# Optimization experiments

Measured on AMD Instinct MI355X. Metric: run time of the kernel, lower is better.

## Reference

```python
import jax, jax.numpy as jnp
import numpy as np
from jax import lax

ROWS, COLS, HID = 5, 5, 4
N = ROWS * COLS
NUM_NEURONS = 128


def _nbr_indices(i, direction):
    # Faithful to get_neighbor_hidden, including the row-wrap behavior of
    # 'col-1'/'col+1' (no column bounds check in the original code).
    row, col = divmod(i, COLS)
    up = (row - 1) * COLS + col
    dn = (row + 1) * COLS + col
    lf = row * COLS + col - 1
    rt = row * COLS + col + 1
    return [up, dn, lf, rt] if direction == 'f' else [up, dn, rt, lf]


def _gather_neighbors(h, idxs):
    # h: (N, bs, HID); returns (bs, 4) of the 4th hidden feature per neighbor
    bs = h.shape[1]
    cols_list = [h[j][:, 3] if 0 <= j < N else jnp.zeros((bs,), h.dtype) for j in idxs]
    return jnp.stack(cols_list, axis=1)


def _make_step(Wx, Wh, Wn, b, direction):
    # One timestep: nodes updated sequentially (node i sees already-updated
    # up/left neighbors within the same timestep, matching the torch loop).
    def step(carry, x_t):  # x_t: (N, bs)
        h, c = carry  # each (N, bs, HID)
        for i in range(N):
            nb = _gather_neighbors(h, _nbr_indices(i, direction))  # (bs,4)
            gates = x_t[i][:, None] @ Wx + h[i] @ Wh + nb @ Wn + b  # (bs,4H)
            ig, fg, og, cc = jnp.split(gates, 4, axis=1)
            nc = jax.nn.sigmoid(fg) * c[i] + jax.nn.sigmoid(ig) * jnp.tanh(cc)
            nh = jax.nn.sigmoid(og) * jnp.tanh(nc)
            h = h.at[i].set(nh)
            c = c.at[i].set(nc)
        return (h, c), None
    return step


def _forward(x, h0f, c0f, h0b, c0b, Wx_f, Wh_f, Wn_f, b_f,
             Wx_b, Wh_b, Wn_b, b_b, W_ff, b_ff, W_out, b_out):
    bs = x.shape[0]
    x_seq = jnp.transpose(x, (2, 1, 0))  # (T, N, bs)
    (hf, cf), _ = lax.scan(_make_step(Wx_f, Wh_f, Wn_f, b_f, 'f'), (h0f, c0f), x_seq)
    (hb, cb), _ = lax.scan(_make_step(Wx_b, Wh_b, Wn_b, b_b, 'b'), (h0b, c0b), x_seq[::-1])
    H_fwd = jnp.transpose(hf, (1, 0, 2))  # (bs, N, HID)
    H_bwd = jnp.transpose(hb, (1, 0, 2))
    H = jnp.concatenate([H_fwd, H_bwd], axis=2).reshape(bs, -1)  # (bs, 200)
    ff = jax.nn.sigmoid(H @ W_ff + b_ff)
    return jax.nn.softmax(ff @ W_out + b_out, axis=1)


def setup_inputs() -> dict:
    key = jax.random.key(0)
    ks = jax.random.split(key, 16)
    bs, T = 8192, 128
    d = {}
    d['x'] = jax.random.normal(ks[0], (bs, N, T), jnp.float32)
    for nm, k in zip(['h0f', 'c0f', 'h0b', 'c0b'], ks[1:5]):
        d[nm] = jax.random.normal(k, (N, bs, HID), jnp.float32) * 0.01
    def lin(k, i, o):
        return jax.random.normal(k, (i, o), jnp.float32) * (1.0 / np.sqrt(i))
    d['Wx_f'] = lin(ks[5], 1, 4 * HID)
    d['Wh_f'] = lin(ks[6], HID, 4 * HID)
    d['Wn_f'] = lin(ks[7], 4, 4 * HID)
    d['b_f'] = jnp.zeros((4 * HID,), jnp.float32)
    d['Wx_b'] = lin(ks[8], 1, 4 * HID)
    d['Wh_b'] = lin(ks[9], HID, 4 * HID)
    d['Wn_b'] = lin(ks[10], 4, 4 * HID)
    d['b_b'] = jnp.zeros((4 * HID,), jnp.float32)
    d['W_ff'] = lin(ks[11], N * 2 * HID, NUM_NEURONS)
    d['b_ff'] = jnp.zeros((NUM_NEURONS,), jnp.float32)
    d['W_out'] = lin(ks[12], NUM_NEURONS, 2)
    d['b_out'] = jnp.zeros((2,), jnp.float32)
    return d


def reference(x, h0f, c0f, h0b, c0b, Wx_f, Wh_f, Wn_f, b_f,
              Wx_b, Wh_b, Wn_b, b_b, W_ff, b_ff, W_out, b_out):
    return _forward(x, h0f, c0f, h0b, c0b, Wx_f, Wh_f, Wn_f, b_f,
                    Wx_b, Wh_b, Wn_b, b_b, W_ff, b_ff, W_out, b_out)
```

## Files before the change

kernel.cpp:

```cpp
#include <hip/hip_runtime.h>
#include <stddef.h>

#define BS 8192
#define NNODE 25
#define TT 128
#define LOG2E 1.4426950408889634f

typedef float v2f __attribute__((ext_vector_type(2)));

__device__ __forceinline__ float ex2(float x) { return __builtin_amdgcn_exp2f(x); }
__device__ __forceinline__ float rcp_(float x) { return __builtin_amdgcn_rcpf(x); }

__device__ float g_xT[(size_t)TT * NNODE * BS];
__device__ float g_hf[NNODE * BS * 4];
__device__ float g_hb[NNODE * BS * 4];

template <int K>
__device__ __forceinline__ float bcast4(float v) {
  int s = __builtin_bit_cast(int, v);
  int r = __builtin_amdgcn_update_dpp(0, s, (K * 0x55), 0xF, 0xF, true);
  return __builtin_bit_cast(float, r);
}

__device__ __forceinline__ void acc2(v2f& A, v2f& B, float s, v2f wa, v2f wb) {
  v2f sv = {s, s};
  A = __builtin_elementwise_fma(sv, wa, A);
  B = __builtin_elementwise_fma(sv, wb, B);
}

__global__ __launch_bounds__(256) void transpose_x(const float* __restrict__ x) {
  __shared__ float tile[32][33];
  const int i = blockIdx.z;
  const int b0 = blockIdx.x * 32;
  const int t0 = blockIdx.y * 32;
  const int tx = threadIdx.x;
  const int ty = threadIdx.y;
#pragma unroll
  for (int j = 0; j < 4; ++j) {
    int bl = ty + j * 8;
    tile[bl][tx] = x[((size_t)(b0 + bl) * NNODE + i) * TT + (t0 + tx)];
  }
  __syncthreads();
#pragma unroll
  for (int j = 0; j < 4; ++j) {
    int tl = ty + j * 8;
    g_xT[((size_t)(t0 + tl) * NNODE + i) * BS + (b0 + tx)] = tile[tx][tl];
  }
}

__global__ __launch_bounds__(256, 1) void rnn_kernel(
    const float* __restrict__ h0f, const float* __restrict__ c0f,
    const float* __restrict__ h0b, const float* __restrict__ c0b,
    const float* __restrict__ Wxf, const float* __restrict__ Whf,
    const float* __restrict__ Wnf, const float* __restrict__ bf,
    const float* __restrict__ Wxb, const float* __restrict__ Whb,
    const float* __restrict__ Wnb, const float* __restrict__ bb_) {
  const int dir = blockIdx.y;
  const int d = threadIdx.x & 3;
  const int b = blockIdx.x * 64 + (threadIdx.x >> 2);

  const float* Wx = dir ? Wxb : Wxf;
  const float* Wh = dir ? Whb : Whf;
  const float* Wn = dir ? Wnb : Wnf;
  const float* Bb = dir ? bb_ : bf;
  const float* h0 = dir ? h0b : h0f;
  const float* c0 = dir ? c0b : c0f;

  const int cI = d, cF = 4 + d, cO = 8 + d, cC = 12 + d;
  const float sS = -LOG2E, sC = 2.0f * LOG2E;

  v2f wA[9], wB[9];
  {
    wA[0] = v2f{sS * Wx[cI], sS * Wx[cF]};
    wB[0] = v2f{sS * Wx[cO], sC * Wx[cC]};
#pragma unroll
    for (int k = 0; k < 4; ++k) {
      wA[1 + k] = v2f{sS * Wh[k * 16 + cI], sS * Wh[k * 16 + cF]};
      wB[1 + k] = v2f{sS * Wh[k * 16 + cO], sC * Wh[k * 16 + cC]};
    }
    const int nrow[4] = {0, 1, dir ? 3 : 2, dir ? 2 : 3};
#pragma unroll
    for (int k = 0; k < 4; ++k) {
      wA[5 + k] = v2f{sS * Wn[nrow[k] * 16 + cI], sS * Wn[nrow[k] * 16 + cF]};
      wB[5 + k] = v2f{sS * Wn[nrow[k] * 16 + cO], sC * Wn[nrow[k] * 16 + cC]};
    }
  }
  const v2f bA = {sS * Bb[cI], sS * Bb[cF]};
  const v2f bB = {sS * Bb[cO], sC * Bb[cC]};

  float h[NNODE], c[NNODE], b3[NNODE];
#pragma unroll
  for (int i = 0; i < NNODE; ++i) {
    h[i] = h0[(i * BS + b) * 4 + d];
    c[i] = c0[(i * BS + b) * 4 + d];
    b3[i] = bcast4<3>(h[i]);
  }

  const float* xbase = g_xT + ((size_t)(dir ? (TT - 1) : 0) * NNODE * BS);
  const ptrdiff_t xstep = dir ? -(ptrdiff_t)(NNODE * BS) : (ptrdiff_t)(NNODE * BS);

  for (int t = 0; t < TT; ++t) {
    float xv[NNODE];
#pragma unroll
    for (int i = 0; i < NNODE; ++i) xv[i] = xbase[(size_t)i * BS + b];

#pragma unroll
    for (int i = 0; i < NNODE; ++i) {
      const float f0 = bcast4<0>(h[i]);
      const float f1 = bcast4<1>(h[i]);
      const float f2 = bcast4<2>(h[i]);

      v2f A = bA, B = bB;
      acc2(A, B, xv[i], wA[0], wB[0]);
      acc2(A, B, f0, wA[1], wB[1]);
      acc2(A, B, f1, wA[2], wB[2]);
      acc2(A, B, f2, wA[3], wB[3]);
      acc2(A, B, b3[i], wA[4], wB[4]);
      if (i >= 5) acc2(A, B, b3[i - 5], wA[5], wB[5]);
      if (i < 20) acc2(A, B, b3[i + 5], wA[6], wB[6]);
      if (i >= 1) acc2(A, B, b3[i - 1], wA[7], wB[7]);
      if (i < 24) acc2(A, B, b3[i + 1], wA[8], wB[8]);

      const float Ei = ex2(A.x);
      const float Ef = ex2(A.y);
      const float Eo = ex2(B.x);
      const float Ec = ex2(B.y);
      const float Di = 1.0f + Ei;
      const float Df = 1.0f + Ef;
      const float P = Di * (Ec + 1.0f);
      const float num = fmaf(c[i], P, (Ec - 1.0f) * Df);
      const float nc = num * rcp_(Df * P);
      const float En = ex2(-2.0f * LOG2E * nc);
      const float hn = (1.0f - En) * rcp_((1.0f + En) * (1.0f + Eo));
      c[i] = nc;
      h[i] = hn;
      b3[i] = bcast4<3>(hn);
    }
    xbase += xstep;
  }

  float* ho = dir ? g_hb : g_hf;
#pragma unroll
  for (int i = 0; i < NNODE; ++i) ho[(i * BS + b) * 4 + d] = h[i];
}

__global__ __launch_bounds__(128) void ff_kernel(
    const float* __restrict__ Wff, const float* __restrict__ bff,
    const float* __restrict__ Wout, const float* __restrict__ bout,
    float* __restrict__ out) {
  __shared__ float Hs[8][200];
  __shared__ float ffs[8][129];
  const int tid = threadIdx.x;
  const int b0 = blockIdx.x * 8;

  for (int idx = tid; idx < 8 * 200; idx += 128) {
    const int bb = idx / 200;
    const int k = idx - bb * 200;
    const int i = k >> 3;
    const int dd = k & 7;
    const int b = b0 + bb;
    Hs[bb][k] = (dd < 4) ? g_hf[(i * BS + b) * 4 + dd]
                         : g_hb[(i * BS + b) * 4 + (dd - 4)];
  }
  __syncthreads();

  float acc[8];
  const float bv = bff[tid];
#pragma unroll
  for (int bb = 0; bb < 8; ++bb) acc[bb] = bv;
  for (int k = 0; k < 200; ++k) {
    const float w = Wff[k * 128 + tid];
#pragma unroll
    for (int bb = 0; bb < 8; ++bb) acc[bb] = fmaf(Hs[bb][k], w, acc[bb]);
  }
#pragma unroll
  for (int bb = 0; bb < 8; ++bb)
    ffs[bb][tid] = rcp_(1.0f + ex2(-LOG2E * acc[bb]));
  __syncthreads();

  if (tid < 8) {
    float z0 = bout[0], z1 = bout[1];
    for (int n = 0; n < 128; ++n) {
      const float f = ffs[tid][n];
      z0 = fmaf(f, Wout[n * 2 + 0], z0);
      z1 = fmaf(f, Wout[n * 2 + 1], z1);
    }
    const float m = fmaxf(z0, z1);
    const float e0 = ex2(LOG2E * (z0 - m)), e1 = ex2(LOG2E * (z1 - m));
    const float s = rcp_(e0 + e1);
    out[(size_t)(b0 + tid) * 2 + 0] = e0 * s;
    out[(size_t)(b0 + tid) * 2 + 1] = e1 * s;
  }
}

extern "C" void kernel_launch(void* const* d_in, const int* in_sizes, int n_in,
                              void* d_out, int out_size, void* d_ws, size_t ws_size,
                              hipStream_t stream) {
  (void)in_sizes; (void)n_in; (void)out_size; (void)d_ws; (void)ws_size;
  const float* x    = (const float*)d_in[0];
  const float* h0f  = (const float*)d_in[1];
  const float* c0f  = (const float*)d_in[2];
  const float* h0b  = (const float*)d_in[3];
  const float* c0b  = (const float*)d_in[4];
  const float* Wxf  = (const float*)d_in[5];
  const float* Whf  = (const float*)d_in[6];
  const float* Wnf  = (const float*)d_in[7];
  const float* bf   = (const float*)d_in[8];
  const float* Wxb  = (const float*)d_in[9];
  const float* Whb  = (const float*)d_in[10];
  const float* Wnb  = (const float*)d_in[11];
  const float* bb   = (const float*)d_in[12];
  const float* Wff  = (const float*)d_in[13];
  const float* bff  = (const float*)d_in[14];
  const float* Wout = (const float*)d_in[15];
  const float* bout = (const float*)d_in[16];
  float* out = (float*)d_out;

  transpose_x<<<dim3(256, 4, 25), dim3(32, 8), 0, stream>>>(x);
  rnn_kernel<<<dim3(128, 2), dim3(256), 0, stream>>>(
      h0f, c0f, h0b, c0b, Wxf, Whf, Wnf, bf, Wxb, Whb, Wnb, bb);
  ff_kernel<<<dim3(1024), dim3(128), 0, stream>>>(Wff, bff, Wout, bout, out);
}
```

Baseline: 590.9 us.

## Drop transpose kernel; read x directly in RNN with paired-timestep vector loads

Removes the separate transpose_x pass and its global scratch buffer, so the RNN kernel reads x in its original (bs, N, T) layout. Each thread loads two consecutive timesteps per node as one float2 and processes two timesteps per outer iteration, with a templated direction. This saves a full read and write of the 105 MB input but makes the RNN loads uncoalesced: the four lanes sharing a batch row hit the same address and neighbouring batch rows are N*T floats apart.

```diff
diff --git a/kernel.cpp b/kernel.cpp
--- a/kernel.cpp
+++ b/kernel.cpp
@@ -11,7 +11,6 @@
 __device__ __forceinline__ float ex2(float x) { return __builtin_amdgcn_exp2f(x); }
 __device__ __forceinline__ float rcp_(float x) { return __builtin_amdgcn_rcpf(x); }
 
-__device__ float g_xT[(size_t)TT * NNODE * BS];
 __device__ float g_hf[NNODE * BS * 4];
 __device__ float g_hb[NNODE * BS * 4];
 
@@ -28,120 +27,108 @@
   B = __builtin_elementwise_fma(sv, wb, B);
 }
 
-__global__ __launch_bounds__(256) void transpose_x(const float* __restrict__ x) {
-  __shared__ float tile[32][33];
-  const int i = blockIdx.z;
-  const int b0 = blockIdx.x * 32;
-  const int t0 = blockIdx.y * 32;
-  const int tx = threadIdx.x;
-  const int ty = threadIdx.y;
-#pragma unroll
-  for (int j = 0; j < 4; ++j) {
-    int bl = ty + j * 8;
-    tile[bl][tx] = x[((size_t)(b0 + bl) * NNODE + i) * TT + (t0 + tx)];
-  }
-  __syncthreads();
-#pragma unroll
-  for (int j = 0; j < 4; ++j) {
-    int tl = ty + j * 8;
-    g_xT[((size_t)(t0 + tl) * NNODE + i) * BS + (b0 + tx)] = tile[tx][tl];
-  }
+template <int DIR>
+__device__ __forceinline__ void rnn_run(
+    int d, int b, const float* __restrict__ x,
+    const float* __restrict__ h0, const float* __restrict__ c0,
+    const float* __restrict__ Wx, const float* __restrict__ Wh,
+    const float* __restrict__ Wn, const float* __restrict__ Bb,
+    float* __restrict__ ho) {
+  const int cI = d, cF = 4 + d, cO = 8 + d, cC = 12 + d;
+  const float sS = -LOG2E, sC = 2.0f * LOG2E;
+
+  v2f wA[9], wB[9];
+  wA[0] = v2f{sS * Wx[cI], sS * Wx[cF]};
+  wB[0] = v2f{sS * Wx[cO], sC * Wx[cC]};
+#pragma unroll
+  for (int k = 0; k < 4; ++k) {
+    wA[1 + k] = v2f{sS * Wh[k * 16 + cI], sS * Wh[k * 16 + cF]};
+    wB[1 + k] = v2f{sS * Wh[k * 16 + cO], sC * Wh[k * 16 + cC]};
+  }
+  const int nrow[4] = {0, 1, DIR ? 3 : 2, DIR ? 2 : 3};
+#pragma unroll
+  for (int k = 0; k < 4; ++k) {
+    wA[5 + k] = v2f{sS * Wn[nrow[k] * 16 + cI], sS * Wn[nrow[k] * 16 + cF]};
+    wB[5 + k] = v2f{sS * Wn[nrow[k] * 16 + cO], sC * Wn[nrow[k] * 16 + cC]};
+  }
+  const v2f bA = {sS * Bb[cI], sS * Bb[cF]};
+  const v2f bB = {sS * Bb[cO], sC * Bb[cC]};
+
+  float h[NNODE], c[NNODE], b3[NNODE];
+#pragma unroll
+  for (int i = 0; i < NNODE; ++i) {
+    h[i] = h0[(i * BS + b) * 4 + d];
+    c[i] = c0[(i * BS + b) * 4 + d];
+    b3[i] = bcast4<3>(h[i]);
+  }
+
+  const float* xrow = x + (size_t)b * (NNODE * TT);
+
+  for (int blk = 0; blk < TT / 2; ++blk) {
+    const int tbase = DIR ? (TT - 2 - 2 * blk) : (2 * blk);
+    v2f xv[NNODE];
+#pragma unroll
+    for (int i = 0; i < NNODE; ++i)
+      xv[i] = *(const v2f*)(xrow + i * TT + tbase);
+
+#pragma unroll
+    for (int k = 0; k < 2; ++k) {
+#pragma unroll
+      for (int i = 0; i < NNODE; ++i) {
+        const float xval =
+            (((DIR ? (1 - k) : k) == 0) ? xv[i].x : xv[i].y);
+        const float f0 = bcast4<0>(h[i]);
+        const float f1 = bcast4<1>(h[i]);
+        const float f2 = bcast4<2>(h[i]);
+
+        v2f A = bA, B = bB;
+        acc2(A, B, xval, wA[0], wB[0]);
+        acc2(A, B, f0, wA[1], wB[1]);
+        acc2(A, B, f1, wA[2], wB[2]);
+        acc2(A, B, f2, wA[3], wB[3]);
+        acc2(A, B, b3[i], wA[4], wB[4]);
+        if (i >= 5) acc2(A, B, b3[i - 5], wA[5], wB[5]);
+        if (i < 20) acc2(A, B, b3[i + 5], wA[6], wB[6]);
+        if (i >= 1) acc2(A, B, b3[i - 1], wA[7], wB[7]);
+        if (i < 24) acc2(A, B, b3[i + 1], wA[8], wB[8]);
+
+        const float Ei = ex2(A.x);
+        const float Ef = ex2(A.y);
+        const float Eo = ex2(B.x);
+        const float Ec = ex2(B.y);
+        const float Di = 1.0f + Ei;
+        const float Df = 1.0f + Ef;
+        const float P = Di * (Ec + 1.0f);
+        const float num = fmaf(c[i], P, (Ec - 1.0f) * Df);
+        const float nc = num * rcp_(Df * P);
+        const float En = ex2(-2.0f * LOG2E * nc);
+        const float hn = (1.0f - En) * rcp_((1.0f + En) * (1.0f + Eo));
+        c[i] = nc;
+        h[i] = hn;
+        b3[i] = bcast4<3>(hn);
+      }
+    }
+  }
+
+#pragma unroll
+  for (int i = 0; i < NNODE; ++i) ho[(i * BS + b) * 4 + d] = h[i];
 }
 
 __global__ __launch_bounds__(256, 1) void rnn_kernel(
+    const float* __restrict__ x,
     const float* __restrict__ h0f, const float* __restrict__ c0f,
     const float* __restrict__ h0b, const float* __restrict__ c0b,
     const float* __restrict__ Wxf, const float* __restrict__ Whf,
     const float* __restrict__ Wnf, const float* __restrict__ bf,
     const float* __restrict__ Wxb, const float* __restrict__ Whb,
     const float* __restrict__ Wnb, const float* __restrict__ bb_) {
-  const int dir = blockIdx.y;
   const int d = threadIdx.x & 3;
   const int b = blockIdx.x * 64 + (threadIdx.x >> 2);
-
-  const float* Wx = dir ? Wxb : Wxf;
-  const float* Wh = dir ? Whb : Whf;
-  const float* Wn = dir ? Wnb : Wnf;
-  const float* Bb = dir ? bb_ : bf;
-  const float* h0 = dir ? h0b : h0f;
-  const float* c0 = dir ? c0b : c0f;
-
-  const int cI = d, cF = 4 + d, cO = 8 + d, cC = 12 + d;
-  const float sS = -LOG2E, sC = 2.0f * LOG2E;
-
-  v2f wA[9], wB[9];
-  {
-    wA[0] = v2f{sS * Wx[cI], sS * Wx[cF]};
-    wB[0] = v2f{sS * Wx[cO], sC * Wx[cC]};
-#pragma unroll
-    for (int k = 0; k < 4; ++k) {
-      wA[1 + k] = v2f{sS * Wh[k * 16 + cI], sS * Wh[k * 16 + cF]};
-      wB[1 + k] = v2f{sS * Wh[k * 16 + cO], sC * Wh[k * 16 + cC]};
-    }
-    const int nrow[4] = {0, 1, dir ? 3 : 2, dir ? 2 : 3};
-#pragma unroll
-    for (int k = 0; k < 4; ++k) {
-      wA[5 + k] = v2f{sS * Wn[nrow[k] * 16 + cI], sS * Wn[nrow[k] * 16 + cF]};
-      wB[5 + k] = v2f{sS * Wn[nrow[k] * 16 + cO], sC * Wn[nrow[k] * 16 + cC]};
-    }
-  }
-  const v2f bA = {sS * Bb[cI], sS * Bb[cF]};
-  const v2f bB = {sS * Bb[cO], sC * Bb[cC]};
-
-  float h[NNODE], c[NNODE], b3[NNODE];
-#pragma unroll
-  for (int i = 0; i < NNODE; ++i) {
-    h[i] = h0[(i * BS + b) * 4 + d];
-    c[i] = c0[(i * BS + b) * 4 + d];
-    b3[i] = bcast4<3>(h[i]);
-  }
-
-  const float* xbase = g_xT + ((size_t)(dir ? (TT - 1) : 0) * NNODE * BS);
-  const ptrdiff_t xstep = dir ? -(ptrdiff_t)(NNODE * BS) : (ptrdiff_t)(NNODE * BS);
-
-  for (int t = 0; t < TT; ++t) {
-    float xv[NNODE];
-#pragma unroll
-    for (int i = 0; i < NNODE; ++i) xv[i] = xbase[(size_t)i * BS + b];
-
-#pragma unroll
-    for (int i = 0; i < NNODE; ++i) {
-      const float f0 = bcast4<0>(h[i]);
-      const float f1 = bcast4<1>(h[i]);
-      const float f2 = bcast4<2>(h[i]);
-
-      v2f A = bA, B = bB;
-      acc2(A, B, xv[i], wA[0], wB[0]);
-      acc2(A, B, f0, wA[1], wB[1]);
-      acc2(A, B, f1, wA[2], wB[2]);
-      acc2(A, B, f2, wA[3], wB[3]);
-      acc2(A, B, b3[i], wA[4], wB[4]);
-      if (i >= 5) acc2(A, B, b3[i - 5], wA[5], wB[5]);
-      if (i < 20) acc2(A, B, b3[i + 5], wA[6], wB[6]);
-      if (i >= 1) acc2(A, B, b3[i - 1], wA[7], wB[7]);
-      if (i < 24) acc2(A, B, b3[i + 1], wA[8], wB[8]);
-
-      const float Ei = ex2(A.x);
-      const float Ef = ex2(A.y);
-      const float Eo = ex2(B.x);
-      const float Ec = ex2(B.y);
-      const float Di = 1.0f + Ei;
-      const float Df = 1.0f + Ef;
-      const float P = Di * (Ec + 1.0f);
-      const float num = fmaf(c[i], P, (Ec - 1.0f) * Df);
-      const float nc = num * rcp_(Df * P);
-      const float En = ex2(-2.0f * LOG2E * nc);
-      const float hn = (1.0f - En) * rcp_((1.0f + En) * (1.0f + Eo));
-      c[i] = nc;
-      h[i] = hn;
-      b3[i] = bcast4<3>(hn);
-    }
-    xbase += xstep;
-  }
-
-  float* ho = dir ? g_hb : g_hf;
-#pragma unroll
-  for (int i = 0; i < NNODE; ++i) ho[(i * BS + b) * 4 + d] = h[i];
+  if (blockIdx.y == 0) {
+    rnn_run<0>(d, b, x, h0f, c0f, Wxf, Whf, Wnf, bf, g_hf);
+  } else {
+    rnn_run<1>(d, b, x, h0b, c0b, Wxb, Whb, Wnb, bb_, g_hb);
+  }
 }
 
 __global__ __launch_bounds__(128) void ff_kernel(
@@ -216,8 +203,7 @@
   const float* bout = (const float*)d_in[16];
   float* out = (float*)d_out;
 
-  transpose_x<<<dim3(256, 4, 25), dim3(32, 8), 0, stream>>>(x);
   rnn_kernel<<<dim3(128, 2), dim3(256), 0, stream>>>(
-      h0f, c0f, h0b, c0b, Wxf, Whf, Wnf, bf, Wxb, Whb, Wnb, bb);
+      x, h0f, c0f, h0b, c0b, Wxf, Whf, Wnf, bf, Wxb, Whb, Wnb, bb);
   ff_kernel<<<dim3(1024), dim3(128), 0, stream>>>(Wff, bff, Wout, bout, out);
 }
```

Measured after the change: 643.0 us. 8.8% more time.
